# Optimization experiments

Measured on AMD Instinct MI355X. Metric: run time of the kernel, lower is better.

## Reference

```python
import jax, jax.numpy as jnp
import numpy as np

B, T, U = 4, 300, 60
ENC_D, DEC_D = 512, 512
INPUT_DIM, INNER_DIM, VOCAB = 1024, 1024, 1000


def setup_inputs() -> dict:
    key = jax.random.key(0)
    ks = jax.random.split(key, 6)
    return {
        "enc_state": jax.random.normal(ks[0], (B, T, ENC_D), dtype=jnp.float32),
        "dec_state": jax.random.normal(ks[1], (B, U, DEC_D), dtype=jnp.float32),
        "W1": jax.random.normal(ks[2], (INPUT_DIM, INNER_DIM), dtype=jnp.float32) * (1.0 / np.sqrt(INPUT_DIM)),
        "b1": jax.random.normal(ks[3], (INNER_DIM,), dtype=jnp.float32) * 0.01,
        "W2": jax.random.normal(ks[4], (INNER_DIM, VOCAB), dtype=jnp.float32) * (1.0 / np.sqrt(INNER_DIM)),
        "b2": jax.random.normal(ks[5], (VOCAB,), dtype=jnp.float32) * 0.01,
    }


def reference(enc_state, dec_state, W1, b1, W2, b2):
    # Original: broadcast enc to (B,T,U,enc_d), dec to (B,T,U,dec_d), concat -> Linear -> tanh -> Linear.
    # Equivalent (same math, no huge concat): split W1 into enc/dec blocks and add broadcasted projections.
    W1_enc, W1_dec = W1[:ENC_D], W1[ENC_D:]
    enc_proj = jnp.einsum('btd,dh->bth', enc_state, W1_enc)  # (B,T,H)
    dec_proj = jnp.einsum('bud,dh->buh', dec_state, W1_dec)  # (B,U,H)
    hidden = jnp.tanh(enc_proj[:, :, None, :] + dec_proj[:, None, :, :] + b1)  # (B,T,U,H)
    logits = jnp.einsum('btuh,hv->btuv', hidden, W2) + b2  # (B,T,U,V)
    return logits
```

## Files before the change

kernel.cpp:

```cpp
#include <hip/hip_runtime.h>
#include <hip/hip_bf16.h>
#include <stdint.h>

#define B_  4
#define T_  300
#define U_  60
#define V_  1000
#define M_TOT (B_*T_*U_)
#define MB_CNT 563
#define WK  1056
#define PK  1040

typedef __attribute__((ext_vector_type(8))) short short8;
typedef __attribute__((ext_vector_type(4))) float f32x4;
typedef __attribute__((ext_vector_type(4))) int int4v;

__device__ __forceinline__ short f2bf(float f) {
    union { float f; uint32_t u; } c; c.f = f;
    uint32_t u = c.u;
    uint32_t r = (u + 0x7FFFu + ((u >> 16) & 1u)) >> 16;
    return (short)r;
}

__device__ __forceinline__ float fast_tanh(float x) {
    float e = __expf(2.0f * x);
    float r = __builtin_amdgcn_rcpf(e + 1.0f);
    return 1.0f - 2.0f * r;
}

__device__ __forceinline__ void gl_lds16(const void* g, void* l) {
    __builtin_amdgcn_global_load_lds(
        (const __attribute__((address_space(1))) void*)g,
        (__attribute__((address_space(3))) void*)l, 16, 0, 0);
}


__global__ void transpose_cvt(const float* __restrict__ in, short* __restrict__ out,
                              int R, int C, int ostride) {
    __shared__ float tile[64][65];
    const int tx = threadIdx.x & 63, ty = threadIdx.x >> 6;
    const int r0 = blockIdx.y * 64, c0 = blockIdx.x * 64;
#pragma unroll
    for (int i = 0; i < 16; ++i) {
        int r = r0 + i * 4 + ty, c = c0 + tx;
        float v = 0.f;
        if (r < R && c < C) v = in[(long)r * C + c];
        tile[i * 4 + ty][tx] = v;
    }
    __syncthreads();
#pragma unroll
    for (int i = 0; i < 16; ++i) {
        int oc = c0 + i * 4 + ty;
        int orr = r0 + tx;
        out[(long)oc * ostride + orr] = f2bf(tile[tx][i * 4 + ty]);
    }
}

__global__ void transpose_pack_w2(const float* __restrict__ in, short* __restrict__ out) {
    __shared__ float tile[64][65];
    const int tx = threadIdx.x & 63, ty = threadIdx.x >> 6;
    const int r0 = blockIdx.y * 64, c0 = blockIdx.x * 64;
#pragma unroll
    for (int i = 0; i < 16; ++i) {
        int r = r0 + i * 4 + ty, c = c0 + tx;
        float v = 0.f;
        if (c < V_) v = in[(long)r * V_ + c];
        tile[i * 4 + ty][tx] = v;
    }
    __syncthreads();
#pragma unroll
    for (int i = 0; i < 16; ++i) {
        int oc = c0 + i * 4 + ty;
        int orr = r0 + tx;
        int nb = oc >> 8, prow = oc & 255, kt = orr >> 5, ks = orr & 31;
        out[(long)(nb * 32 + kt) * 8192 + prow * 32 + ks] = f2bf(tile[tx][i * 4 + ty]);
    }
}

__global__ __launch_bounds__(256, 2) void proj_gemm(
        const float* __restrict__ X, int M, int k_off,
        const short* __restrict__ Wt,
        const float* __restrict__ b1,
        float* __restrict__ P)
{
    __shared__ short As[64 * 64];
    const int tid = threadIdx.x;
    const int lane = tid & 63;
    const int w = tid >> 6;
    const int wm = w >> 1, wn = w & 1;
    const int m0 = blockIdx.x * 64, n0 = blockIdx.y * 64;

    f32x4 acc[2][2] = {};
    for (int k0 = 0; k0 < 512; k0 += 64) {
#pragma unroll
        for (int c = 0; c < 2; ++c) {
            int lin = tid + 256 * c;
            int row = lin >> 3, k8 = lin & 7;
            int m = m0 + row;
            short vals[8];
            if (m < M) {
                const float* xp = X + (long)m * 512 + k0 + k8 * 8;
#pragma unroll
                for (int j = 0; j < 8; ++j) vals[j] = f2bf(xp[j]);
            } else {
#pragma unroll
                for (int j = 0; j < 8; ++j) vals[j] = 0;
            }
            int byte = row * 128 + k8 * 16;
            byte ^= (row & 7) << 4;
            *(int4v*)((char*)As + byte) = *(const int4v*)vals;
        }
        __syncthreads();
#pragma unroll
        for (int ks = 0; ks < 2; ++ks) {
            short8 af[2];
#pragma unroll
            for (int mf = 0; mf < 2; ++mf) {
                int row = wm * 32 + mf * 16 + (lane & 15);
                int byte = row * 128 + ks * 64 + (lane >> 4) * 16;
                byte ^= (row & 7) << 4;
                af[mf] = *(const short8*)((char*)As + byte);
            }
#pragma unroll
            for (int nf = 0; nf < 2; ++nf) {
                int h = n0 + wn * 32 + nf * 16 + (lane & 15);
                const short* bp = Wt + (long)h * WK + k_off + k0 + ks * 32 + (lane >> 4) * 8;
                short8 bfv = *(const short8*)bp;
#pragma unroll
                for (int mf = 0; mf < 2; ++mf)
                    acc[mf][nf] = __builtin_amdgcn_mfma_f32_16x16x32_bf16(af[mf], bfv, acc[mf][nf], 0, 0, 0);
            }
        }
        __syncthreads();
    }
#pragma unroll
    for (int mf = 0; mf < 2; ++mf)
#pragma unroll
        for (int nf = 0; nf < 2; ++nf) {
            int h = n0 + wn * 32 + nf * 16 + (lane & 15);
            float bb = b1 ? b1[h] : 0.f;
#pragma unroll
            for (int j = 0; j < 4; ++j) {
                int m = m0 + wm * 32 + mf * 16 + (lane >> 4) * 4 + j;
                if (m < M) P[(long)m * PK + h] = acc[mf][nf][j] + bb;
            }
        }
}

__global__ __launch_bounds__(256) void hgen_pk(
        const float* __restrict__ encP, const float* __restrict__ decP,
        short* __restrict__ Hp)
{
    long idx = (long)blockIdx.x * 256 + threadIdx.x;
    int u = (int)(idx >> 9);
    int gi = (int)(idx & 511);
    int mb = u >> 5, kt = u & 31;
    int r = gi >> 2, g = gi & 3;
    int m = mb * 128 + r;
    int k = kt * 32 + g * 8;
    short8 v = {};
    if (m < M_TOT) {
        int bt = m / U_;
        int uu = m - bt * U_;
        int b = m / (T_ * U_);
        const float* e = encP + (long)bt * PK + k;
        const float* d = decP + (long)(b * U_ + uu) * PK + k;
        f32x4 e0 = *(const f32x4*)(e), e1 = *(const f32x4*)(e + 4);
        f32x4 d0 = *(const f32x4*)(d), d1 = *(const f32x4*)(d + 4);
#pragma unroll
        for (int j = 0; j < 4; ++j) v[j]     = f2bf(fast_tanh(e0[j] + d0[j]));
#pragma unroll
        for (int j = 0; j < 4; ++j) v[4 + j] = f2bf(fast_tanh(e1[j] + d1[j]));
    }
    *(short8*)(Hp + (long)u * 4096 + gi * 8) = v;
}

__global__ __launch_bounds__(512, 4) void gemm_pk(
        const short* __restrict__ Hp,
        const short* __restrict__ W2p,
        const float* __restrict__ b2,
        float* __restrict__ out)
{
    __shared__ __align__(16) char lds[3 * 24576];

    const int tid = threadIdx.x;
    const int lane = tid & 63;
    const int w = tid >> 6;
    const int wm = w >> 2, wn = w & 3;
    const int l15 = lane & 15, ksel = lane >> 4;

    const int nwg = gridDim.x;
    int bid = blockIdx.x;
    int q = nwg >> 3, r = nwg & 7;
    int xcd = bid & 7, lq = bid >> 3;
    int wg = (xcd < r ? xcd * (q + 1) : r * (q + 1) + (xcd - r) * q) + lq;
    const int mb = wg >> 2;
    const int nb = wg & 3;
    const int m0 = mb * 128, n0 = nb * 256;

    const int sr = tid >> 2;
    const int sg = (tid & 3) ^ ((sr >> 1) & 3);
    const short* aU = Hp + (long)mb * 32 * 4096 + sr * 32 + sg * 8;
    const short* bU = W2p + (long)nb * 32 * 8192 + sr * 32 + sg * 8;
    char* const ldsw = (char*)lds + (w << 10);

#define STAGE_A(t_, sl_) gl_lds16(aU + (long)(t_) * 4096, ldsw + (sl_) * 24576)
#define STAGE_B(t_, sl_) do {                                               \
    char* db_ = ldsw + (sl_) * 24576 + 8192;                                \
    gl_lds16(bU + (long)(t_) * 8192, db_);                                  \
    gl_lds16(bU + (long)(t_) * 8192 + 4096, db_ + 8192);                    \
} while (0)

    f32x4 acc[4][4] = {};
    short8 af[4], bf[4];

#define PH_A(sl_, DOSTAGE, t2_, ss_) do {                                   \
    const char* Ab_ = (const char*)lds + (sl_) * 24576;                     \
    const char* Bb_ = Ab_ + 8192;                                           \
    _Pragma("unroll")                                                       \
    for (int nf = 0; nf < 2; ++nf) {                                        \
        int rw = wn * 64 + nf * 16 + l15;                                   \
        bf[nf] = *(const short8*)(Bb_ + rw * 64 + ((ksel ^ ((rw >> 1) & 3)) << 4)); \
    }                                                                       \
    _Pragma("unroll")                                                       \
    for (int mf = 0; mf < 4; ++mf) {                                        \
        int rw = wm * 64 + mf * 16 + l15;                                   \
        af[mf] = *(const short8*)(Ab_ + rw * 64 + ((ksel ^ ((rw >> 1) & 3)) << 4)); \
    }                                                                       \
    if (DOSTAGE) STAGE_A(t2_, ss_);                                         \
    __builtin_amdgcn_s_barrier();                                           \
    asm volatile("s_waitcnt lgkmcnt(0)" ::: "memory");                      \
    __builtin_amdgcn_s_setprio(1);                                          \
    _Pragma("unroll")                                                       \
    for (int nf = 0; nf < 2; ++nf)                                          \
        _Pragma("unroll")                                                   \
        for (int mf = 0; mf < 4; ++mf)                                      \
            acc[mf][nf] = __builtin_amdgcn_mfma_f32_16x16x32_bf16(          \
                af[mf], bf[nf], acc[mf][nf], 0, 0, 0);                      \
    __builtin_amdgcn_s_setprio(0);                                          \
    __builtin_amdgcn_s_barrier();                                           \
} while (0)

#define PH_B(sl_, DOSTAGE, t2_, ss_, GATE) do {                             \
    const char* Ab_ = (const char*)lds + (sl_) * 24576;                     \
    const char* Bb_ = Ab_ + 8192;                                           \
    _Pragma("unroll")                                                       \
    for (int nf = 2; nf < 4; ++nf) {                                        \
        int rw = wn * 64 + nf * 16 + l15;                                   \
        bf[nf] = *(const short8*)(Bb_ + rw * 64 + ((ksel ^ ((rw >> 1) & 3)) << 4)); \
    }                                                                       \
    if (DOSTAGE) STAGE_B(t2_, ss_);                                         \
    GATE                                                                    \
    __builtin_amdgcn_s_barrier();                                           \
    asm volatile("s_waitcnt lgkmcnt(0)" ::: "memory");                      \
    __builtin_amdgcn_s_setprio(1);                                          \
    _Pragma("unroll")                                                       \
    for (int nf = 2; nf < 4; ++nf)                                          \
        _Pragma("unroll")                                                   \
        for (int mf = 0; mf < 4; ++mf)                                      \
            acc[mf][nf] = __builtin_amdgcn_mfma_f32_16x16x32_bf16(          \
                af[mf], bf[nf], acc[mf][nf], 0, 0, 0);                      \
    __builtin_amdgcn_s_setprio(0);                                          \
    __builtin_amdgcn_s_barrier();                                           \
} while (0)

#define GATE3 asm volatile("s_waitcnt vmcnt(3)" ::: "memory");
#define GATE0 asm volatile("s_waitcnt vmcnt(0)" ::: "memory");
#define NOGATE

    STAGE_A(0, 0); STAGE_B(0, 0);
    STAGE_A(1, 1); STAGE_B(1, 1);
    asm volatile("s_waitcnt vmcnt(3)" ::: "memory");
    __builtin_amdgcn_s_barrier();

    int s = 0, ss = 2;
#pragma unroll 1
    for (int t = 0; t < 30; ++t) {
        PH_A(s, true, t + 2, ss);
        PH_B(s, true, t + 2, ss, GATE3);
        s = (s == 2) ? 0 : s + 1;
        ss = (ss == 2) ? 0 : ss + 1;
    }
    PH_A(s, false, 0, 0); PH_B(s, false, 0, 0, GATE0);
    s = (s == 2) ? 0 : s + 1;
    PH_A(s, false, 0, 0); PH_B(s, false, 0, 0, NOGATE);

#pragma unroll
    for (int nf = 0; nf < 4; ++nf) {
        int n = n0 + wn * 64 + nf * 16 + l15;
        if (n < V_) {
            float bv = b2[n];
#pragma unroll
            for (int mf = 0; mf < 4; ++mf)
#pragma unroll
                for (int j = 0; j < 4; ++j) {
                    int m = m0 + wm * 64 + mf * 16 + ksel * 4 + j;
                    if (m < M_TOT)
                        out[(long)m * V_ + n] = acc[mf][nf][j] + bv;
                }
        }
    }
#undef PH_A
#undef PH_B
#undef STAGE_A
#undef STAGE_B
#undef GATE3
#undef GATE0
#undef NOGATE
}

__global__ __launch_bounds__(512, 2) void joint_gemm(
        const float* __restrict__ encP, const float* __restrict__ decP,
        const short* __restrict__ W2t, const float* __restrict__ b2,
        float* __restrict__ out)
{
    __shared__ short As[2][64 * 64];
    const int tid = threadIdx.x;
    const int lane = tid & 63;
    const int w = tid >> 6;
    const int m0 = blockIdx.x * 64;
    const int n0 = blockIdx.y * 512;

    const int arow = tid >> 3;
    const int k8 = tid & 7;
    const int am = m0 + arow;
    const int bt = am / U_;
    const int u = am - bt * U_;
    const int bidx = am / (T_ * U_);
    const float* eptr = encP + (long)bt * PK + k8 * 8;
    const float* dptr = decP + (long)(bidx * U_ + u) * PK + k8 * 8;
    const int wbyte = (arow * 128 + k8 * 16) ^ ((arow & 7) << 4);

    f32x4 acc[4][4] = {};
    const short* bbase[4];
#pragma unroll
    for (int nf = 0; nf < 4; ++nf) {
        int n = n0 + w * 64 + nf * 16 + (lane & 15);
        bbase[nf] = W2t + (long)n * WK + (lane >> 4) * 8;
    }
    f32x4 e0 = *(const f32x4*)(eptr), e1 = *(const f32x4*)(eptr + 4);
    f32x4 d0 = *(const f32x4*)(dptr), d1 = *(const f32x4*)(dptr + 4);
    {
        short vals[8];
#pragma unroll
        for (int j = 0; j < 4; ++j) vals[j]     = f2bf(fast_tanh(e0[j] + d0[j]));
#pragma unroll
        for (int j = 0; j < 4; ++j) vals[4 + j] = f2bf(fast_tanh(e1[j] + d1[j]));
        *(int4v*)((char*)&As[0][0] + wbyte) = *(const int4v*)vals;
    }
    e0 = *(const f32x4*)(eptr + 64); e1 = *(const f32x4*)(eptr + 68);
    d0 = *(const f32x4*)(dptr + 64); d1 = *(const f32x4*)(dptr + 68);
    asm volatile("s_waitcnt lgkmcnt(0)" ::: "memory");
    __builtin_amdgcn_s_barrier();

#pragma unroll 1
    for (int t = 0; t < 16; ++t) {
        const int k0 = t * 64;
        short8 bfr[2][4];
#pragma unroll
        for (int ks = 0; ks < 2; ++ks)
#pragma unroll
            for (int nf = 0; nf < 4; ++nf)
                bfr[ks][nf] = *(const short8*)(bbase[nf] + k0 + ks * 32);
        if (t < 15) {
            short vals[8];
#pragma unroll
            for (int j = 0; j < 4; ++j) vals[j]     = f2bf(fast_tanh(e0[j] + d0[j]));
#pragma unroll
            for (int j = 0; j < 4; ++j) vals[4 + j] = f2bf(fast_tanh(e1[j] + d1[j]));
            *(int4v*)((char*)&As[(t & 1) ^ 1][0] + wbyte) = *(const int4v*)vals;
            if (t < 14) {
                e0 = *(const f32x4*)(eptr + k0 + 128); e1 = *(const f32x4*)(eptr + k0 + 132);
                d0 = *(const f32x4*)(dptr + k0 + 128); d1 = *(const f32x4*)(dptr + k0 + 132);
            }
        }
        const char* rb = (const char*)&As[t & 1][0];
#pragma unroll
        for (int ks = 0; ks < 2; ++ks) {
            short8 af[4];
#pragma unroll
            for (int mf = 0; mf < 4; ++mf) {
                int row = mf * 16 + (lane & 15);
                int byte = (row * 128 + ks * 64 + (lane >> 4) * 16) ^ ((row & 7) << 4);
                af[mf] = *(const short8*)(rb + byte);
            }
#pragma unroll
            for (int nf = 0; nf < 4; ++nf)
#pragma unroll
                for (int mf = 0; mf < 4; ++mf)
                    acc[mf][nf] = __builtin_amdgcn_mfma_f32_16x16x32_bf16(
                        af[mf], bfr[ks][nf], acc[mf][nf], 0, 0, 0);
        }
        if (t < 15) {
            asm volatile("s_waitcnt lgkmcnt(0)" ::: "memory");
            __builtin_amdgcn_s_barrier();
        }
    }
#pragma unroll
    for (int nf = 0; nf < 4; ++nf) {
        int n = n0 + w * 64 + nf * 16 + (lane & 15);
        float bv = (n < V_) ? b2[n] : 0.f;
#pragma unroll
        for (int mf = 0; mf < 4; ++mf)
#pragma unroll
            for (int j = 0; j < 4; ++j) {
                int m = m0 + mf * 16 + (lane >> 4) * 4 + j;
                if (n < V_)
                    out[(long)m * V_ + n] = acc[mf][nf][j] + bv;
            }
    }
}

extern "C" void kernel_launch(void* const* d_in, const int* in_sizes, int n_in,
                              void* d_out, int out_size, void* d_ws, size_t ws_size,
                              hipStream_t stream) {
    const float* enc = (const float*)d_in[0];
    const float* dec = (const float*)d_in[1];
    const float* W1  = (const float*)d_in[2];
    const float* b1  = (const float*)d_in[3];
    const float* W2  = (const float*)d_in[4];
    const float* b2  = (const float*)d_in[5];
    float* out = (float*)d_out;

    char* ws = (char*)d_ws;
    size_t off = 0;
    short* W1t  = (short*)(ws + off); off += (size_t)1024 * WK * 2;
    short* W2p  = (short*)(ws + off); off += (size_t)4 * 32 * 8192 * 2;
    float* encP = (float*)(ws + off); off += (size_t)1200 * PK * 4;
    float* decP = (float*)(ws + off); off += (size_t)240 * PK * 4;
    short* Hp   = (short*)(ws + off);
    size_t need = off + (size_t)MB_CNT * 32 * 4096 * 2;

    transpose_cvt<<<dim3(16, 16), 256, 0, stream>>>(W1, W1t, 1024, 1024, WK);
    proj_gemm<<<dim3(19, 16), 256, 0, stream>>>(enc, 1200, 0,   W1t, nullptr, encP);
    proj_gemm<<<dim3(4, 16),  256, 0, stream>>>(dec, 240,  512, W1t, b1,      decP);

    if (ws_size >= need) {
        transpose_pack_w2<<<dim3(16, 16), 256, 0, stream>>>(W2, W2p);
        hgen_pk<<<MB_CNT * 32 * 512 / 256, 256, 0, stream>>>(encP, decP, Hp);
        gemm_pk<<<MB_CNT * 4, 512, 0, stream>>>(Hp, W2p, b2, out);
    } else {
        short* W2t = W2p;
        transpose_cvt<<<dim3(16, 16), 256, 0, stream>>>(W2, W2t, 1024, 1000, WK);
        joint_gemm<<<dim3(1125, 2), 512, 0, stream>>>(encP, decP, W2t, b2, out);
    }
}
```

Baseline: 362.4 us.

## Enlarge joint GEMM tile to 256x256 with 64-deep K and double-buffered LDS

Replaces the 128x256 output tile GEMM (K step 32, triple-buffered) with a 256x256 tile using 64-wide K slices. The H and W2 packing layouts are changed to match, with half-tile sub-blocks and an XOR swizzle over 128-byte rows. The goal is more arithmetic per byte loaded and fewer barriers per FLOP. In exchange it uses 128KB of LDS and many more accumulator registers, which drops occupancy to 2 workgroups per CU and leaves fewer, larger blocks, so tail and wave-quantization effects get worse.

```diff
diff --git a/kernel.cpp b/kernel.cpp
--- a/kernel.cpp
+++ b/kernel.cpp
@@ -7,7 +7,7 @@
 #define U_  60
 #define V_  1000
 #define M_TOT (B_*T_*U_)
-#define MB_CNT 563
+#define MBCNT 282
 #define WK  1056
 #define PK  1040
 
@@ -72,8 +72,10 @@
     for (int i = 0; i < 16; ++i) {
         int oc = c0 + i * 4 + ty;
         int orr = r0 + tx;
-        int nb = oc >> 8, prow = oc & 255, kt = orr >> 5, ks = orr & 31;
-        out[(long)(nb * 32 + kt) * 8192 + prow * 32 + ks] = f2bf(tile[tx][i * 4 + ty]);
+        int nb = oc >> 8, pr = oc & 255, h = pr >> 7, rr = pr & 127;
+        int t = orr >> 6, kk = orr & 63;
+        out[(long)((nb * 16 + t) * 2 + h) * 8192 + rr * 64 + kk] =
+            f2bf(tile[tx][i * 4 + ty]);
     }
 }
 
@@ -152,12 +154,12 @@
         short* __restrict__ Hp)
 {
     long idx = (long)blockIdx.x * 256 + threadIdx.x;
-    int u = (int)(idx >> 9);
-    int gi = (int)(idx & 511);
-    int mb = u >> 5, kt = u & 31;
-    int r = gi >> 2, g = gi & 3;
-    int m = mb * 128 + r;
-    int k = kt * 32 + g * 8;
+    int u = (int)(idx >> 10);
+    int gi = (int)(idx & 1023);
+    int mb = u >> 5, rem = u & 31, t = rem >> 1, h = rem & 1;
+    int r = gi >> 3, kg = gi & 7;
+    int m = mb * 256 + h * 128 + r;
+    int k = t * 64 + kg * 8;
     short8 v = {};
     if (m < M_TOT) {
         int bt = m / U_;
@@ -172,16 +174,16 @@
 #pragma unroll
         for (int j = 0; j < 4; ++j) v[4 + j] = f2bf(fast_tanh(e1[j] + d1[j]));
     }
-    *(short8*)(Hp + (long)u * 4096 + gi * 8) = v;
-}
-
-__global__ __launch_bounds__(512, 4) void gemm_pk(
+    *(short8*)(Hp + (long)u * 8192 + gi * 8) = v;
+}
+
+__global__ __launch_bounds__(512, 2) void gemm8p(
         const short* __restrict__ Hp,
         const short* __restrict__ W2p,
         const float* __restrict__ b2,
         float* __restrict__ out)
 {
-    __shared__ __align__(16) char lds[3 * 24576];
+    __shared__ __align__(16) char lds[131072];
 
     const int tid = threadIdx.x;
     const int lane = tid & 63;
@@ -194,119 +196,160 @@
     int q = nwg >> 3, r = nwg & 7;
     int xcd = bid & 7, lq = bid >> 3;
     int wg = (xcd < r ? xcd * (q + 1) : r * (q + 1) + (xcd - r) * q) + lq;
-    const int mb = wg >> 2;
-    const int nb = wg & 3;
-    const int m0 = mb * 128, n0 = nb * 256;
-
-    const int sr = tid >> 2;
-    const int sg = (tid & 3) ^ ((sr >> 1) & 3);
-    const short* aU = Hp + (long)mb * 32 * 4096 + sr * 32 + sg * 8;
-    const short* bU = W2p + (long)nb * 32 * 8192 + sr * 32 + sg * 8;
-    char* const ldsw = (char*)lds + (w << 10);
-
-#define STAGE_A(t_, sl_) gl_lds16(aU + (long)(t_) * 4096, ldsw + (sl_) * 24576)
-#define STAGE_B(t_, sl_) do {                                               \
-    char* db_ = ldsw + (sl_) * 24576 + 8192;                                \
-    gl_lds16(bU + (long)(t_) * 8192, db_);                                  \
-    gl_lds16(bU + (long)(t_) * 8192 + 4096, db_ + 8192);                    \
+    const int mb = wg >> 2, nb = wg & 3;
+
+    const int rowA = tid >> 3;
+    const int gA = (tid & 7) ^ (rowA & 7);
+    const short* aSrc = Hp  + (long)mb * 262144 + rowA * 64 + gA * 8;
+    const short* bSrc = W2p + (long)nb * 262144 + rowA * 64 + gA * 8;
+    const int wq = w << 10;
+
+#define ST_A(uidx_, roff_) do {                                              \
+    gl_lds16(aSrc + (long)(uidx_) * 8192, (char*)lds + (roff_) + wq);        \
+    gl_lds16(aSrc + (long)(uidx_) * 8192 + 4096,                             \
+             (char*)lds + (roff_) + 8192 + wq);                              \
 } while (0)
-
-    f32x4 acc[4][4] = {};
-    short8 af[4], bf[4];
-
-#define PH_A(sl_, DOSTAGE, t2_, ss_) do {                                   \
-    const char* Ab_ = (const char*)lds + (sl_) * 24576;                     \
-    const char* Bb_ = Ab_ + 8192;                                           \
-    _Pragma("unroll")                                                       \
-    for (int nf = 0; nf < 2; ++nf) {                                        \
-        int rw = wn * 64 + nf * 16 + l15;                                   \
-        bf[nf] = *(const short8*)(Bb_ + rw * 64 + ((ksel ^ ((rw >> 1) & 3)) << 4)); \
-    }                                                                       \
-    _Pragma("unroll")                                                       \
-    for (int mf = 0; mf < 4; ++mf) {                                        \
-        int rw = wm * 64 + mf * 16 + l15;                                   \
-        af[mf] = *(const short8*)(Ab_ + rw * 64 + ((ksel ^ ((rw >> 1) & 3)) << 4)); \
-    }                                                                       \
-    if (DOSTAGE) STAGE_A(t2_, ss_);                                         \
-    __builtin_amdgcn_s_barrier();                                           \
-    asm volatile("s_waitcnt lgkmcnt(0)" ::: "memory");                      \
-    __builtin_amdgcn_s_setprio(1);                                          \
-    _Pragma("unroll")                                                       \
-    for (int nf = 0; nf < 2; ++nf)                                          \
-        _Pragma("unroll")                                                   \
-        for (int mf = 0; mf < 4; ++mf)                                      \
-            acc[mf][nf] = __builtin_amdgcn_mfma_f32_16x16x32_bf16(          \
-                af[mf], bf[nf], acc[mf][nf], 0, 0, 0);                      \
-    __builtin_amdgcn_s_setprio(0);                                          \
-    __builtin_amdgcn_s_barrier();                                           \
+#define ST_B(uidx_, roff_) do {                                              \
+    gl_lds16(bSrc + (long)(uidx_) * 8192, (char*)lds + (roff_) + wq);        \
+    gl_lds16(bSrc + (long)(uidx_) * 8192 + 4096,                             \
+             (char*)lds + (roff_) + 8192 + wq);                              \
 } while (0)
 
-#define PH_B(sl_, DOSTAGE, t2_, ss_, GATE) do {                             \
-    const char* Ab_ = (const char*)lds + (sl_) * 24576;                     \
-    const char* Bb_ = Ab_ + 8192;                                           \
-    _Pragma("unroll")                                                       \
-    for (int nf = 2; nf < 4; ++nf) {                                        \
-        int rw = wn * 64 + nf * 16 + l15;                                   \
-        bf[nf] = *(const short8*)(Bb_ + rw * 64 + ((ksel ^ ((rw >> 1) & 3)) << 4)); \
-    }                                                                       \
-    if (DOSTAGE) STAGE_B(t2_, ss_);                                         \
-    GATE                                                                    \
-    __builtin_amdgcn_s_barrier();                                           \
-    asm volatile("s_waitcnt lgkmcnt(0)" ::: "memory");                      \
-    __builtin_amdgcn_s_setprio(1);                                          \
-    _Pragma("unroll")                                                       \
-    for (int nf = 2; nf < 4; ++nf)                                          \
-        _Pragma("unroll")                                                   \
-        for (int mf = 0; mf < 4; ++mf)                                      \
-            acc[mf][nf] = __builtin_amdgcn_mfma_f32_16x16x32_bf16(          \
-                af[mf], bf[nf], acc[mf][nf], 0, 0, 0);                      \
-    __builtin_amdgcn_s_setprio(0);                                          \
-    __builtin_amdgcn_s_barrier();                                           \
+    short8 af[4][2], bf0[2][2], bf1[2][2];
+    f32x4 acc[8][4] = {};
+
+#define RD_AF(d_, qm_) do {                                                  \
+    _Pragma("unroll")                                                        \
+    for (int mf = 0; mf < 4; ++mf) {                                         \
+        const int rw_ = wm * 64 + mf * 16 + l15;                             \
+        const char* bp_ = (const char*)lds + (d_) * 65536 + (qm_) * 16384    \
+                          + rw_ * 128;                                       \
+        const int sx_ = (rw_ & 7) << 4;                                      \
+        af[mf][0] = *(const short8*)(bp_ + ((ksel * 16) ^ sx_));             \
+        af[mf][1] = *(const short8*)(bp_ + ((64 + ksel * 16) ^ sx_));        \
+    } } while (0)
+
+#define RD_BF(d_, qn_, B_) do {                                              \
+    _Pragma("unroll")                                                        \
+    for (int nf = 0; nf < 2; ++nf) {                                         \
+        const int rw_ = wn * 32 + nf * 16 + l15;                             \
+        const char* bp_ = (const char*)lds + (d_) * 65536 + 32768            \
+                          + (qn_) * 16384 + rw_ * 128;                       \
+        const int sx_ = (rw_ & 7) << 4;                                      \
+        B_[nf][0] = *(const short8*)(bp_ + ((ksel * 16) ^ sx_));             \
+        B_[nf][1] = *(const short8*)(bp_ + ((64 + ksel * 16) ^ sx_));        \
+    } } while (0)
+
+#define MM(qm_, qn_, B_) do {                                                \
+    __builtin_amdgcn_s_setprio(1);                                           \
+    _Pragma("unroll")                                                        \
+    for (int kh = 0; kh < 2; ++kh)                                           \
+        _Pragma("unroll")                                                    \
+        for (int nf = 0; nf < 2; ++nf)                                       \
+            _Pragma("unroll")                                                \
+            for (int mf = 0; mf < 4; ++mf)                                   \
+                acc[(qm_) * 4 + mf][(qn_) * 2 + nf] =                        \
+                    __builtin_amdgcn_mfma_f32_16x16x32_bf16(                 \
+                        af[mf][kh], B_[nf][kh],                              \
+                        acc[(qm_) * 4 + mf][(qn_) * 2 + nf], 0, 0, 0);       \
+    __builtin_amdgcn_s_setprio(0);                                           \
 } while (0)
 
-#define GATE3 asm volatile("s_waitcnt vmcnt(3)" ::: "memory");
-#define GATE0 asm volatile("s_waitcnt vmcnt(0)" ::: "memory");
-#define NOGATE
-
-    STAGE_A(0, 0); STAGE_B(0, 0);
-    STAGE_A(1, 1); STAGE_B(1, 1);
-    asm volatile("s_waitcnt vmcnt(3)" ::: "memory");
-    __builtin_amdgcn_s_barrier();
-
-    int s = 0, ss = 2;
+#define GATE(n_) asm volatile("s_waitcnt vmcnt(" #n_ ")" ::: "memory")
+#define BARC do {                                                            \
+    __builtin_amdgcn_s_barrier();                                            \
+    asm volatile("s_waitcnt lgkmcnt(0)" ::: "memory");                       \
+    __builtin_amdgcn_sched_barrier(0);                                       \
+} while (0)
+#define BARE __builtin_amdgcn_s_barrier()
+
+#define TILE(t_, c_, n_, G3_) do {                                           \
+                                                     \
+    RD_AF(c_, 0); RD_BF(c_, 0, bf0);                                         \
+    ST_B(((t_) + 1) * 2,     (n_) * 65536 + 32768);                          \
+    GATE(6);                                                                 \
+    asm volatile("s_waitcnt lgkmcnt(8)" ::: "memory");                       \
+    BARC; MM(0, 0, bf0); BARE;                                               \
+                                                              \
+    RD_BF(c_, 1, bf1);                                                       \
+    ST_B(((t_) + 1) * 2 + 1, (n_) * 65536 + 49152);                          \
+    GATE(6);                                                                 \
+    BARC; MM(0, 1, bf1); BARE;                                               \
+                                                              \
+    RD_AF(c_, 1);                                                            \
+    ST_A(((t_) + 1) * 2 + 1, (n_) * 65536 + 16384);                          \
+    BARC; MM(1, 0, bf0); BARE;                                               \
+                                                              \
+    ST_A(((t_) + 2) * 2,     (c_) * 65536);                                  \
+    G3_;                                                                     \
+    BARC; MM(1, 1, bf1); BARE;                                               \
+} while (0)
+
+    ST_A(0, 0);
+    ST_B(0, 32768);
+    ST_B(1, 49152);
+    ST_A(1, 16384);
+    ST_A(2, 65536);
+    GATE(6);
+    BARE;
+
 #pragma unroll 1
-    for (int t = 0; t < 30; ++t) {
-        PH_A(s, true, t + 2, ss);
-        PH_B(s, true, t + 2, ss, GATE3);
-        s = (s == 2) ? 0 : s + 1;
-        ss = (ss == 2) ? 0 : ss + 1;
-    }
-    PH_A(s, false, 0, 0); PH_B(s, false, 0, 0, GATE0);
-    s = (s == 2) ? 0 : s + 1;
-    PH_A(s, false, 0, 0); PH_B(s, false, 0, 0, NOGATE);
-
-#pragma unroll
-    for (int nf = 0; nf < 4; ++nf) {
-        int n = n0 + wn * 64 + nf * 16 + l15;
-        if (n < V_) {
-            float bv = b2[n];
-#pragma unroll
-            for (int mf = 0; mf < 4; ++mf)
-#pragma unroll
-                for (int j = 0; j < 4; ++j) {
-                    int m = m0 + wm * 64 + mf * 16 + ksel * 4 + j;
-                    if (m < M_TOT)
-                        out[(long)m * V_ + n] = acc[mf][nf][j] + bv;
-                }
-        }
-    }
-#undef PH_A
-#undef PH_B
-#undef STAGE_A
-#undef STAGE_B
-#undef GATE3
-#undef GATE0
-#undef NOGATE
+    for (int tt = 0; tt < 14; tt += 2) {
+        TILE(tt,     0, 1, GATE(6));
+        TILE(tt + 1, 1, 0, GATE(6));
+    }
+    RD_AF(0, 0); RD_BF(0, 0, bf0);
+    ST_B(30, 65536 + 32768);
+    GATE(6);
+    asm volatile("s_waitcnt lgkmcnt(8)" ::: "memory");
+    BARC; MM(0, 0, bf0); BARE;
+    RD_BF(0, 1, bf1);
+    ST_B(31, 65536 + 49152);
+    GATE(6);
+    BARC; MM(0, 1, bf1); BARE;
+    RD_AF(0, 1);
+    ST_A(31, 65536 + 16384);
+    BARC; MM(1, 0, bf0); BARE;
+    GATE(4);
+    BARC; MM(1, 1, bf1); BARE;
+    RD_AF(1, 0); RD_BF(1, 0, bf0);
+    GATE(2);
+    BARC; MM(0, 0, bf0); BARE;
+    RD_BF(1, 1, bf1);
+    GATE(0);
+    BARC; MM(0, 1, bf1); BARE;
+    RD_AF(1, 1);
+    BARC; MM(1, 0, bf0); BARE;
+    BARC; MM(1, 1, bf1);
+
+#pragma unroll
+    for (int qn = 0; qn < 2; ++qn)
+#pragma unroll
+        for (int nf = 0; nf < 2; ++nf) {
+            int n = nb * 256 + qn * 128 + wn * 32 + nf * 16 + l15;
+            if (n < V_) {
+                float bv = b2[n];
+#pragma unroll
+                for (int qm = 0; qm < 2; ++qm)
+#pragma unroll
+                    for (int mf = 0; mf < 4; ++mf)
+#pragma unroll
+                        for (int j = 0; j < 4; ++j) {
+                            int m = mb * 256 + qm * 128 + wm * 64 + mf * 16 + ksel * 4 + j;
+                            if (m < M_TOT)
+                                out[(long)m * V_ + n] = acc[qm * 4 + mf][qn * 2 + nf][j] + bv;
+                        }
+            }
+        }
+#undef ST_A
+#undef ST_B
+#undef RD_AF
+#undef RD_BF
+#undef MM
+#undef GATE
+#undef BARC
+#undef BARE
+#undef TILE
 }
 
 __global__ __launch_bounds__(512, 2) void joint_gemm(
@@ -425,11 +468,11 @@
     char* ws = (char*)d_ws;
     size_t off = 0;
     short* W1t  = (short*)(ws + off); off += (size_t)1024 * WK * 2;
-    short* W2p  = (short*)(ws + off); off += (size_t)4 * 32 * 8192 * 2;
+    short* W2p  = (short*)(ws + off); off += (size_t)1024 * WK * 2;
     float* encP = (float*)(ws + off); off += (size_t)1200 * PK * 4;
     float* decP = (float*)(ws + off); off += (size_t)240 * PK * 4;
     short* Hp   = (short*)(ws + off);
-    size_t need = off + (size_t)MB_CNT * 32 * 4096 * 2;
+    size_t need = off + (size_t)MBCNT * 262144 * 2;
 
     transpose_cvt<<<dim3(16, 16), 256, 0, stream>>>(W1, W1t, 1024, 1024, WK);
     proj_gemm<<<dim3(19, 16), 256, 0, stream>>>(enc, 1200, 0,   W1t, nullptr, encP);
@@ -437,8 +480,8 @@
 
     if (ws_size >= need) {
         transpose_pack_w2<<<dim3(16, 16), 256, 0, stream>>>(W2, W2p);
-        hgen_pk<<<MB_CNT * 32 * 512 / 256, 256, 0, stream>>>(encP, decP, Hp);
-        gemm_pk<<<MB_CNT * 4, 512, 0, stream>>>(Hp, W2p, b2, out);
+        hgen_pk<<<MBCNT * 32 * 1024 / 256, 256, 0, stream>>>(encP, decP, Hp);
+        gemm8p<<<MBCNT * 4, 512, 0, stream>>>(Hp, W2p, b2, out);
     } else {
         short* W2t = W2p;
         transpose_cvt<<<dim3(16, 16), 256, 0, stream>>>(W2, W2t, 1024, 1000, WK);
```

After: 339.7 us. -6.3%, faster.

## Merge prep and projection launches, store projections as bf16, drop fallback path

Applied to the files above, without the earlier changes.

Combines the W1 and W2 transpose kernels into one launch via a z-dimension switch and merges the encoder and decoder projection GEMMs into one grid. The projection outputs are now stored as bf16 instead of padded fp32, which halves the bytes hgen_pk reads. The workspace-size fallback joint_gemm path is removed. Rounding the pre-tanh sums to bf16 adds some error, and the code now assumes the workspace is always large enough.

```diff
diff --git a/kernel.cpp b/kernel.cpp
--- a/kernel.cpp
+++ b/kernel.cpp
@@ -9,7 +9,6 @@
 #define M_TOT (B_*T_*U_)
 #define MB_CNT 563
 #define WK  1056
-#define PK  1040
 
 typedef __attribute__((ext_vector_type(8))) short short8;
 typedef __attribute__((ext_vector_type(4))) float f32x4;
@@ -22,6 +21,12 @@
     return (short)r;
 }
 
+__device__ __forceinline__ float b2f(short s) {
+    union { float f; uint32_t u; } c;
+    c.u = ((uint32_t)(uint16_t)s) << 16;
+    return c.f;
+}
+
 __device__ __forceinline__ float fast_tanh(float x) {
     float e = __expf(2.0f * x);
     float r = __builtin_amdgcn_rcpf(e + 1.0f);
@@ -34,61 +39,62 @@
         (__attribute__((address_space(3))) void*)l, 16, 0, 0);
 }
 
-
-__global__ void transpose_cvt(const float* __restrict__ in, short* __restrict__ out,
-                              int R, int C, int ostride) {
+__global__ void prep_weights(const float* __restrict__ W1, const float* __restrict__ W2,
+                             short* __restrict__ W1t, short* __restrict__ W2p) {
     __shared__ float tile[64][65];
     const int tx = threadIdx.x & 63, ty = threadIdx.x >> 6;
     const int r0 = blockIdx.y * 64, c0 = blockIdx.x * 64;
-#pragma unroll
-    for (int i = 0; i < 16; ++i) {
-        int r = r0 + i * 4 + ty, c = c0 + tx;
-        float v = 0.f;
-        if (r < R && c < C) v = in[(long)r * C + c];
-        tile[i * 4 + ty][tx] = v;
-    }
-    __syncthreads();
-#pragma unroll
-    for (int i = 0; i < 16; ++i) {
-        int oc = c0 + i * 4 + ty;
-        int orr = r0 + tx;
-        out[(long)oc * ostride + orr] = f2bf(tile[tx][i * 4 + ty]);
-    }
-}
-
-__global__ void transpose_pack_w2(const float* __restrict__ in, short* __restrict__ out) {
-    __shared__ float tile[64][65];
-    const int tx = threadIdx.x & 63, ty = threadIdx.x >> 6;
-    const int r0 = blockIdx.y * 64, c0 = blockIdx.x * 64;
-#pragma unroll
-    for (int i = 0; i < 16; ++i) {
-        int r = r0 + i * 4 + ty, c = c0 + tx;
-        float v = 0.f;
-        if (c < V_) v = in[(long)r * V_ + c];
-        tile[i * 4 + ty][tx] = v;
-    }
-    __syncthreads();
-#pragma unroll
-    for (int i = 0; i < 16; ++i) {
-        int oc = c0 + i * 4 + ty;
-        int orr = r0 + tx;
-        int nb = oc >> 8, prow = oc & 255, kt = orr >> 5, ks = orr & 31;
-        out[(long)(nb * 32 + kt) * 8192 + prow * 32 + ks] = f2bf(tile[tx][i * 4 + ty]);
-    }
-}
-
-__global__ __launch_bounds__(256, 2) void proj_gemm(
-        const float* __restrict__ X, int M, int k_off,
-        const short* __restrict__ Wt,
-        const float* __restrict__ b1,
-        float* __restrict__ P)
+    if (blockIdx.z == 0) {
+#pragma unroll
+        for (int i = 0; i < 16; ++i) {
+            int r = r0 + i * 4 + ty, c = c0 + tx;
+            tile[i * 4 + ty][tx] = W1[(long)r * 1024 + c];
+        }
+        __syncthreads();
+#pragma unroll
+        for (int i = 0; i < 16; ++i) {
+            int oc = c0 + i * 4 + ty;
+            int orr = r0 + tx;
+            W1t[(long)oc * WK + orr] = f2bf(tile[tx][i * 4 + ty]);
+        }
+    } else {
+#pragma unroll
+        for (int i = 0; i < 16; ++i) {
+            int r = r0 + i * 4 + ty, c = c0 + tx;
+            float v = 0.f;
+            if (c < V_) v = W2[(long)r * V_ + c];
+            tile[i * 4 + ty][tx] = v;
+        }
+        __syncthreads();
+#pragma unroll
+        for (int i = 0; i < 16; ++i) {
+            int oc = c0 + i * 4 + ty;
+            int orr = r0 + tx;
+            int nb = oc >> 8, prow = oc & 255, kt = orr >> 5, ks = orr & 31;
+            W2p[(long)(nb * 32 + kt) * 8192 + prow * 32 + ks] = f2bf(tile[tx][i * 4 + ty]);
+        }
+    }
+}
+
+__global__ __launch_bounds__(256, 2) void proj_both(
+        const float* __restrict__ enc, const float* __restrict__ dec,
+        const short* __restrict__ Wt, const float* __restrict__ b1,
+        short* __restrict__ encB, short* __restrict__ decB)
 {
     __shared__ short As[64 * 64];
     const int tid = threadIdx.x;
     const int lane = tid & 63;
     const int w = tid >> 6;
     const int wm = w >> 1, wn = w & 1;
-    const int m0 = blockIdx.x * 64, n0 = blockIdx.y * 64;
+
+    const int bx = blockIdx.x;
+    const bool isenc = bx < 19;
+    const float* X  = isenc ? enc : dec;
+    const int M     = isenc ? 1200 : 240;
+    const int k_off = isenc ? 0 : 512;
+    short* P        = isenc ? encB : decB;
+    const int m0 = (isenc ? bx : bx - 19) * 64;
+    const int n0 = blockIdx.y * 64;
 
     f32x4 acc[2][2] = {};
     for (int k0 = 0; k0 < 512; k0 += 64) {
@@ -138,17 +144,17 @@
 #pragma unroll
         for (int nf = 0; nf < 2; ++nf) {
             int h = n0 + wn * 32 + nf * 16 + (lane & 15);
-            float bb = b1 ? b1[h] : 0.f;
+            float bb = isenc ? 0.f : b1[h];
 #pragma unroll
             for (int j = 0; j < 4; ++j) {
                 int m = m0 + wm * 32 + mf * 16 + (lane >> 4) * 4 + j;
-                if (m < M) P[(long)m * PK + h] = acc[mf][nf][j] + bb;
+                if (m < M) P[(long)m * 1024 + h] = f2bf(acc[mf][nf][j] + bb);
             }
         }
 }
 
 __global__ __launch_bounds__(256) void hgen_pk(
-        const float* __restrict__ encP, const float* __restrict__ decP,
+        const short* __restrict__ encB, const short* __restrict__ decB,
         short* __restrict__ Hp)
 {
     long idx = (long)blockIdx.x * 256 + threadIdx.x;
@@ -163,14 +169,11 @@
         int bt = m / U_;
         int uu = m - bt * U_;
         int b = m / (T_ * U_);
-        const float* e = encP + (long)bt * PK + k;
-        const float* d = decP + (long)(b * U_ + uu) * PK + k;
-        f32x4 e0 = *(const f32x4*)(e), e1 = *(const f32x4*)(e + 4);
-        f32x4 d0 = *(const f32x4*)(d), d1 = *(const f32x4*)(d + 4);
-#pragma unroll
-        for (int j = 0; j < 4; ++j) v[j]     = f2bf(fast_tanh(e0[j] + d0[j]));
-#pragma unroll
-        for (int j = 0; j < 4; ++j) v[4 + j] = f2bf(fast_tanh(e1[j] + d1[j]));
+        short8 e = *(const short8*)(encB + (long)bt * 1024 + k);
+        short8 d = *(const short8*)(decB + (long)(b * U_ + uu) * 1024 + k);
+#pragma unroll
+        for (int j = 0; j < 8; ++j)
+            v[j] = f2bf(fast_tanh(b2f(e[j]) + b2f(d[j])));
     }
     *(short8*)(Hp + (long)u * 4096 + gi * 8) = v;
 }
@@ -307,108 +310,6 @@
 #undef GATE3
 #undef GATE0
 #undef NOGATE
-}
-
-__global__ __launch_bounds__(512, 2) void joint_gemm(
-        const float* __restrict__ encP, const float* __restrict__ decP,
-        const short* __restrict__ W2t, const float* __restrict__ b2,
-        float* __restrict__ out)
-{
-    __shared__ short As[2][64 * 64];
-    const int tid = threadIdx.x;
-    const int lane = tid & 63;
-    const int w = tid >> 6;
-    const int m0 = blockIdx.x * 64;
-    const int n0 = blockIdx.y * 512;
-
-    const int arow = tid >> 3;
-    const int k8 = tid & 7;
-    const int am = m0 + arow;
-    const int bt = am / U_;
-    const int u = am - bt * U_;
-    const int bidx = am / (T_ * U_);
-    const float* eptr = encP + (long)bt * PK + k8 * 8;
-    const float* dptr = decP + (long)(bidx * U_ + u) * PK + k8 * 8;
-    const int wbyte = (arow * 128 + k8 * 16) ^ ((arow & 7) << 4);
-
-    f32x4 acc[4][4] = {};
-    const short* bbase[4];
-#pragma unroll
-    for (int nf = 0; nf < 4; ++nf) {
-        int n = n0 + w * 64 + nf * 16 + (lane & 15);
-        bbase[nf] = W2t + (long)n * WK + (lane >> 4) * 8;
-    }
-    f32x4 e0 = *(const f32x4*)(eptr), e1 = *(const f32x4*)(eptr + 4);
-    f32x4 d0 = *(const f32x4*)(dptr), d1 = *(const f32x4*)(dptr + 4);
-    {
-        short vals[8];
-#pragma unroll
-        for (int j = 0; j < 4; ++j) vals[j]     = f2bf(fast_tanh(e0[j] + d0[j]));
-#pragma unroll
-        for (int j = 0; j < 4; ++j) vals[4 + j] = f2bf(fast_tanh(e1[j] + d1[j]));
-        *(int4v*)((char*)&As[0][0] + wbyte) = *(const int4v*)vals;
-    }
-    e0 = *(const f32x4*)(eptr + 64); e1 = *(const f32x4*)(eptr + 68);
-    d0 = *(const f32x4*)(dptr + 64); d1 = *(const f32x4*)(dptr + 68);
-    asm volatile("s_waitcnt lgkmcnt(0)" ::: "memory");
-    __builtin_amdgcn_s_barrier();
-
-#pragma unroll 1
-    for (int t = 0; t < 16; ++t) {
-        const int k0 = t * 64;
-        short8 bfr[2][4];
-#pragma unroll
-        for (int ks = 0; ks < 2; ++ks)
-#pragma unroll
-            for (int nf = 0; nf < 4; ++nf)
-                bfr[ks][nf] = *(const short8*)(bbase[nf] + k0 + ks * 32);
-        if (t < 15) {
-            short vals[8];
-#pragma unroll
-            for (int j = 0; j < 4; ++j) vals[j]     = f2bf(fast_tanh(e0[j] + d0[j]));
-#pragma unroll
-            for (int j = 0; j < 4; ++j) vals[4 + j] = f2bf(fast_tanh(e1[j] + d1[j]));
-            *(int4v*)((char*)&As[(t & 1) ^ 1][0] + wbyte) = *(const int4v*)vals;
-            if (t < 14) {
-                e0 = *(const f32x4*)(eptr + k0 + 128); e1 = *(const f32x4*)(eptr + k0 + 132);
-                d0 = *(const f32x4*)(dptr + k0 + 128); d1 = *(const f32x4*)(dptr + k0 + 132);
-            }
-        }
-        const char* rb = (const char*)&As[t & 1][0];
-#pragma unroll
-        for (int ks = 0; ks < 2; ++ks) {
-            short8 af[4];
-#pragma unroll
-            for (int mf = 0; mf < 4; ++mf) {
-                int row = mf * 16 + (lane & 15);
-                int byte = (row * 128 + ks * 64 + (lane >> 4) * 16) ^ ((row & 7) << 4);
-                af[mf] = *(const short8*)(rb + byte);
-            }
-#pragma unroll
-            for (int nf = 0; nf < 4; ++nf)
-#pragma unroll
-                for (int mf = 0; mf < 4; ++mf)
-                    acc[mf][nf] = __builtin_amdgcn_mfma_f32_16x16x32_bf16(
-                        af[mf], bfr[ks][nf], acc[mf][nf], 0, 0, 0);
-        }
-        if (t < 15) {
-            asm volatile("s_waitcnt lgkmcnt(0)" ::: "memory");
-            __builtin_amdgcn_s_barrier();
-        }
-    }
-#pragma unroll
-    for (int nf = 0; nf < 4; ++nf) {
-        int n = n0 + w * 64 + nf * 16 + (lane & 15);
-        float bv = (n < V_) ? b2[n] : 0.f;
-#pragma unroll
-        for (int mf = 0; mf < 4; ++mf)
-#pragma unroll
-            for (int j = 0; j < 4; ++j) {
-                int m = m0 + mf * 16 + (lane >> 4) * 4 + j;
-                if (n < V_)
-                    out[(long)m * V_ + n] = acc[mf][nf][j] + bv;
-            }
-    }
 }
 
 extern "C" void kernel_launch(void* const* d_in, const int* in_sizes, int n_in,
@@ -426,22 +327,12 @@
     size_t off = 0;
     short* W1t  = (short*)(ws + off); off += (size_t)1024 * WK * 2;
     short* W2p  = (short*)(ws + off); off += (size_t)4 * 32 * 8192 * 2;
-    float* encP = (float*)(ws + off); off += (size_t)1200 * PK * 4;
-    float* decP = (float*)(ws + off); off += (size_t)240 * PK * 4;
+    short* encB = (short*)(ws + off); off += (size_t)1216 * 1024 * 2;
+    short* decB = (short*)(ws + off); off += (size_t)256 * 1024 * 2;
     short* Hp   = (short*)(ws + off);
-    size_t need = off + (size_t)MB_CNT * 32 * 4096 * 2;
-
-    transpose_cvt<<<dim3(16, 16), 256, 0, stream>>>(W1, W1t, 1024, 1024, WK);
-    proj_gemm<<<dim3(19, 16), 256, 0, stream>>>(enc, 1200, 0,   W1t, nullptr, encP);
-    proj_gemm<<<dim3(4, 16),  256, 0, stream>>>(dec, 240,  512, W1t, b1,      decP);
-
-    if (ws_size >= need) {
-        transpose_pack_w2<<<dim3(16, 16), 256, 0, stream>>>(W2, W2p);
-        hgen_pk<<<MB_CNT * 32 * 512 / 256, 256, 0, stream>>>(encP, decP, Hp);
-        gemm_pk<<<MB_CNT * 4, 512, 0, stream>>>(Hp, W2p, b2, out);
-    } else {
-        short* W2t = W2p;
-        transpose_cvt<<<dim3(16, 16), 256, 0, stream>>>(W2, W2t, 1024, 1000, WK);
-        joint_gemm<<<dim3(1125, 2), 512, 0, stream>>>(encP, decP, W2t, b2, out);
-    }
-}
+
+    prep_weights<<<dim3(16, 16, 2), 256, 0, stream>>>(W1, W2, W1t, W2p);
+    proj_both<<<dim3(23, 16), 256, 0, stream>>>(enc, dec, W1t, b1, encB, decB);
+    hgen_pk<<<MB_CNT * 32 * 512 / 256, 256, 0, stream>>>(encB, decB, Hp);
+    gemm_pk<<<MB_CNT * 4, 512, 0, stream>>>(Hp, W2p, b2, out);
+}
```

Measured after the change: 331.0 us. 8.7% less time.
